# Kernel tuning notes

Hardware: AMD Instinct MI355X
Metric: run time of the kernel (lower is better)

Reference implementation:

```python
import jax, jax.numpy as jnp
import numpy as np

N_EMBED = 4096
N_Q_HEADS = 32
N_KV_HEADS = 8
HEAD_DIM = N_EMBED // N_Q_HEADS  # 128
N_GROUPS = N_Q_HEADS // N_KV_HEADS  # 4
ROPE_BASE = 10000.0
BATCH, SEQ = 1, 2048


def setup_inputs() -> dict:
    key = jax.random.key(0)
    ks = jax.random.split(key, 5)
    hidden_state = jax.random.normal(ks[0], (BATCH, SEQ, N_EMBED), dtype=jnp.float32)
    # additive causal mask: 0 on/below diagonal, -inf above (SDPA float-mask semantics)
    causal = jnp.tril(jnp.ones((SEQ, SEQ), dtype=bool))
    attention_mask = jnp.where(causal, 0.0, -jnp.inf).astype(jnp.float32)[None, None]
    position_ids = jnp.arange(SEQ, dtype=jnp.int32)[None, :].repeat(BATCH, axis=0)
    s = 0.02
    Wq = jax.random.normal(ks[1], (N_EMBED, N_EMBED), dtype=jnp.float32) * s
    Wk = jax.random.normal(ks[2], (N_KV_HEADS * HEAD_DIM, N_EMBED), dtype=jnp.float32) * s
    Wv = jax.random.normal(ks[3], (N_KV_HEADS * HEAD_DIM, N_EMBED), dtype=jnp.float32) * s
    Wo = jax.random.normal(ks[4], (N_EMBED, N_EMBED), dtype=jnp.float32) * s
    return {"hidden_state": hidden_state, "attention_mask": attention_mask,
            "position_ids": position_ids, "Wq": Wq, "Wk": Wk, "Wv": Wv, "Wo": Wo}


def _rope_tables(position_ids):
    # mimic torch: inv_freq built in fp16 then used as float
    exponent = (jnp.arange(0, HEAD_DIM, 2, dtype=jnp.float16) / HEAD_DIM)
    inv_freq = (1.0 / (ROPE_BASE ** exponent)).astype(jnp.float32)  # [hd/2]
    m = position_ids.astype(jnp.float32)  # [bs, seq]
    m_theta = m[:, :, None] * inv_freq[None, None, :]  # [bs, seq, hd/2]
    m_theta = jnp.concatenate([m_theta, m_theta], axis=-1)  # [bs, seq, hd]
    return jnp.cos(m_theta), jnp.sin(m_theta)


def _rotate_half(x):
    half = x.shape[-1] // 2
    return jnp.concatenate([-x[..., half:], x[..., :half]], axis=-1)


def reference(hidden_state, attention_mask, position_ids, Wq, Wk, Wv, Wo):
    bs, seq, _ = hidden_state.shape
    q = (hidden_state @ Wq.T).reshape(bs, seq, N_Q_HEADS, HEAD_DIM).transpose(0, 2, 1, 3)
    k = (hidden_state @ Wk.T).reshape(bs, seq, N_KV_HEADS, HEAD_DIM).transpose(0, 2, 1, 3)
    v = (hidden_state @ Wv.T).reshape(bs, seq, N_KV_HEADS, HEAD_DIM).transpose(0, 2, 1, 3)

    cos, sin = _rope_tables(position_ids)
    cos, sin = cos[:, None], sin[:, None]  # broadcast over heads
    q = q * cos + _rotate_half(q) * sin
    k = k * cos + _rotate_half(k) * sin

    # GQA: group query heads per KV head instead of materializing KV copies
    qg = q.reshape(bs, N_KV_HEADS, N_GROUPS, seq, HEAD_DIM)
    scale = 1.0 / jnp.sqrt(jnp.float32(HEAD_DIM))
    scores = jnp.einsum('bhgqd,bhkd->bhgqk', qg, k) * scale + attention_mask[:, :, None]
    probs = jax.nn.softmax(scores, axis=-1)
    attn = jnp.einsum('bhgqk,bhkd->bhgqd', probs, v)  # [bs, kvh, g, seq, hd]
    attn = attn.reshape(bs, N_Q_HEADS, seq, HEAD_DIM).transpose(0, 2, 1, 3).reshape(bs, seq, N_EMBED)
    return attn @ Wo.T
```

## Files before the change

### kernel.cpp

```cpp
#include <hip/hip_runtime.h>
#include <hip/hip_bf16.h>

#define SEQ 2048
#define LDQKV 6144

typedef __attribute__((ext_vector_type(8))) __bf16 bf16x8;
typedef __attribute__((ext_vector_type(4))) __bf16 bf16x4;
typedef __attribute__((ext_vector_type(4))) float f32x4;

__device__ __forceinline__ void gload_lds16(const void* g, void* l) {
  __builtin_amdgcn_global_load_lds((__attribute__((address_space(1))) void*)(g),
                                   (__attribute__((address_space(3))) void*)(l), 16, 0, 0);
}

struct CvtArgs {
  const float* src0; const float* src1; const float* src2; const float* src3; const float* src4;
  __bf16* dst0; __bf16* dst1; __bf16* dst2; __bf16* dst3; __bf16* dst4;
};
__global__ __launch_bounds__(256) void cvt_all(CvtArgs a) {
  int b = blockIdx.x;
  const float* s; __bf16* d; int boff;
  if (b < 8192)       { s = a.src0; d = a.dst0; boff = b; }
  else if (b < 24576) { s = a.src1; d = a.dst1; boff = b - 8192; }
  else if (b < 28672) { s = a.src2; d = a.dst2; boff = b - 24576; }
  else if (b < 32768) { s = a.src3; d = a.dst3; boff = b - 28672; }
  else                { s = a.src4; d = a.dst4; boff = b - 32768; }
  long i = ((long)boff * 256 + threadIdx.x) * 4;
  f32x4 v = *(const f32x4*)(s + i);
  bf16x4 o;
  #pragma unroll
  for (int j = 0; j < 4; ++j) o[j] = (__bf16)v[j];
  *(bf16x4*)(d + i) = o;
}

__global__ __launch_bounds__(256) void rope_tab_k(const int* __restrict__ pos,
                                                  float* __restrict__ tab) {
  int i = blockIdx.x * 256 + threadIdx.x;
  int s = i >> 6, j = i & 63;
  float p = (float)pos[s];
  float pw = powf(10000.0f, (float)j * (1.0f / 64.0f));
  _Float16 ph = (_Float16)pw;
  _Float16 ivh = (_Float16)(1.0f / (float)ph);
  float freq = (float)ivh;
  float th = p * freq;
  tab[i] = cosf(th);
  tab[SEQ * 64 + i] = sinf(th);
}

__global__ __launch_bounds__(256) void rope_apply_k(__bf16* __restrict__ qkv,
                                                    const float* __restrict__ tab) {
  int i = blockIdx.x * 256 + threadIdx.x;
  int dc = i & 7;
  int ht = (i >> 3) % 40;
  int s = i / 320;
  long col = (ht < 32) ? (long)ht * 128 : (long)4096 + (long)(ht - 32) * 128;
  __bf16* p = qkv + (long)s * LDQKV + col + dc * 8;
  bf16x8 lo = *(bf16x8*)p;
  bf16x8 hi = *(bf16x8*)(p + 64);
  const float* tc = tab + (long)s * 64 + dc * 8;
  const float* ts = tc + SEQ * 64;
  bf16x8 lo2, hi2;
  #pragma unroll
  for (int e = 0; e < 8; ++e) {
    float c = tc[e], sn = ts[e];
    float lv = (float)lo[e], hv = (float)hi[e];
    lo2[e] = (__bf16)(lv * c - hv * sn);
    hi2[e] = (__bf16)(hv * c + lv * sn);
  }
  *(bf16x8*)p = lo2;
  *(bf16x8*)(p + 64) = hi2;
}

template <bool OUT_BF16>
__global__ __launch_bounds__(256) void gemm_nt(const __bf16* __restrict__ A,
                                               const __bf16* __restrict__ B,
                                               void* __restrict__ C,
                                               int K, int ldc) {
  __shared__ __align__(16) __bf16 Al[8192];
  __shared__ __align__(16) __bf16 Bl[8192];
  const int tid = threadIdx.x;
  const int wave = tid >> 6, lane = tid & 63;
  const int l15 = lane & 15, l4 = lane >> 4;
  const int brow = blockIdx.x * 128, bcol = blockIdx.y * 128;
  const int wm = wave >> 1, wn = wave & 1;

  f32x4 acc[4][4] = {};

  for (int k0 = 0; k0 < K; k0 += 64) {
    __syncthreads();
    #pragma unroll
    for (int i = 0; i < 4; ++i) {
      int fo = i * 2048 + wave * 512 + lane * 8;
      int r = fo >> 6, c = fo & 63;
      int cs = c ^ ((r & 7) << 3);
      gload_lds16(A + (long)(brow + r) * K + k0 + cs, &Al[i * 2048 + wave * 512]);
      gload_lds16(B + (long)(bcol + r) * K + k0 + cs, &Bl[i * 2048 + wave * 512]);
    }
    __syncthreads();
    #pragma unroll
    for (int ks = 0; ks < 2; ++ks) {
      bf16x8 af[4], bfr[4];
      #pragma unroll
      for (int mi = 0; mi < 4; ++mi) {
        int r = wm * 64 + mi * 16 + l15;
        int c = ks * 32 + l4 * 8;
        af[mi] = *(const bf16x8*)&Al[r * 64 + (c ^ ((r & 7) << 3))];
      }
      #pragma unroll
      for (int ni = 0; ni < 4; ++ni) {
        int r = wn * 64 + ni * 16 + l15;
        int c = ks * 32 + l4 * 8;
        bfr[ni] = *(const bf16x8*)&Bl[r * 64 + (c ^ ((r & 7) << 3))];
      }
      #pragma unroll
      for (int mi = 0; mi < 4; ++mi)
        #pragma unroll
        for (int ni = 0; ni < 4; ++ni)
          acc[mi][ni] = __builtin_amdgcn_mfma_f32_16x16x32_bf16(af[mi], bfr[ni], acc[mi][ni], 0, 0, 0);
    }
  }
  #pragma unroll
  for (int mi = 0; mi < 4; ++mi)
    #pragma unroll
    for (int ni = 0; ni < 4; ++ni)
      #pragma unroll
      for (int j = 0; j < 4; ++j) {
        long rr = brow + wm * 64 + mi * 16 + l4 * 4 + j;
        long cc = bcol + wn * 64 + ni * 16 + l15;
        float v = acc[mi][ni][j];
        if (OUT_BF16) ((__bf16*)C)[rr * ldc + cc] = (__bf16)v;
        else          ((float*)C)[rr * ldc + cc] = v;
      }
}

__global__ __launch_bounds__(256) void flash_k(const __bf16* __restrict__ qkv,
                                               __bf16* __restrict__ ctx) {
  __shared__ __align__(16) __bf16 Kl[8192];
  __shared__ __align__(16) __bf16 Vt[8192];
  __shared__ __align__(16) __bf16 Pl[4][1024];

  const int bid = blockIdx.x;
  const int h = bid & 31;
  const int qt = 31 - (bid >> 5);
  const int kvh = h >> 2;
  const int q0 = qt * 64;
  const int tid = threadIdx.x, wave = tid >> 6, lane = tid & 63;
  const int l15 = lane & 15, l4 = lane >> 4;
  const int d2 = tid & 63, grp = tid >> 6;

  const __bf16* Qp = qkv + (long)h * 128;
  const __bf16* Kp = qkv + 4096 + (long)kvh * 128;
  const __bf16* Vp = qkv + 5120 + (long)kvh * 128;

  bf16x8 aq[4];
  {
    long qr = q0 + wave * 16 + l15;
    #pragma unroll
    for (int ks = 0; ks < 4; ++ks)
      aq[ks] = *(const bf16x8*)(Qp + qr * LDQKV + ks * 32 + l4 * 8);
  }
  f32x4 accO[8] = {};
  float lsum[4] = {0.f, 0.f, 0.f, 0.f};
  const float cexp = 0.08838834764831845f * 1.4426950408889634f;

  for (int kv0 = 0; kv0 <= q0; kv0 += 64) {
    __syncthreads();
    #pragma unroll
    for (int i = 0; i < 4; ++i) {
      int fo = i * 2048 + wave * 512 + lane * 8;
      int r = fo >> 7, c = fo & 127;
      int cs = c ^ ((r & 7) << 3);
      gload_lds16(Kp + (long)(kv0 + r) * LDQKV + cs, &Kl[i * 2048 + wave * 512]);
    }
    unsigned int vv[2][8];
    #pragma unroll
    for (int rep = 0; rep < 2; ++rep) {
      int cch = grp * 2 + rep;
      #pragma unroll
      for (int i = 0; i < 8; ++i)
        vv[rep][i] = *(const unsigned int*)(Vp + (long)(kv0 + cch * 8 + i) * LDQKV + 2 * d2);
    }
    #pragma unroll
    for (int rep = 0; rep < 2; ++rep) {
      int cch = grp * 2 + rep;
      #pragma unroll
      for (int half = 0; half < 2; ++half) {
        bf16x8 w;
        #pragma unroll
        for (int i = 0; i < 8; ++i)
          w[i] = __builtin_bit_cast(__bf16, (unsigned short)(vv[rep][i] >> (16 * half)));
        int d = 2 * d2 + half;
        *(bf16x8*)&Vt[d * 64 + ((cch * 8) ^ ((d2 & 7) * 8))] = w;
      }
    }
    __syncthreads();

    f32x4 s[4];
    #pragma unroll
    for (int t = 0; t < 4; ++t) s[t] = f32x4{0.f, 0.f, 0.f, 0.f};
    __builtin_amdgcn_s_setprio(1);
    #pragma unroll
    for (int t = 0; t < 4; ++t) {
      int r = t * 16 + l15;
      #pragma unroll
      for (int ks = 0; ks < 4; ++ks) {
        bf16x8 bk = *(const bf16x8*)&Kl[r * 128 + ((ks * 32 + l4 * 8) ^ ((r & 7) << 3))];
        s[t] = __builtin_amdgcn_mfma_f32_16x16x32_bf16(aq[ks], bk, s[t], 0, 0, 0);
      }
    }
    __builtin_amdgcn_s_setprio(0);

    const bool lastStep = (kv0 == q0);
    float pout[4][4];
    #pragma unroll
    for (int t = 0; t < 4; ++t)
      #pragma unroll
      for (int j = 0; j < 4; ++j) {
        float p = exp2f(s[t][j] * cexp);
        if (lastStep) {
          int qg = wave * 16 + l4 * 4 + j;
          int kg = t * 16 + l15;
          if (kg > qg) p = 0.f;
        }
        pout[t][j] = p;
      }
    #pragma unroll
    for (int j = 0; j < 4; ++j)
      lsum[j] += (pout[0][j] + pout[1][j]) + (pout[2][j] + pout[3][j]);

    #pragma unroll
    for (int t = 0; t < 4; ++t)
      #pragma unroll
      for (int j = 0; j < 4; ++j) {
        int r = l4 * 4 + j;
        int c = t * 16 + l15;
        Pl[wave][r * 64 + (c ^ ((r & 7) << 3))] = (__bf16)pout[t][j];
      }
    asm volatile("s_waitcnt lgkmcnt(0)" ::: "memory");
    __builtin_amdgcn_sched_barrier(0);
    bf16x8 ap[2];
    #pragma unroll
    for (int ks2 = 0; ks2 < 2; ++ks2) {
      int c = ks2 * 32 + l4 * 8;
      ap[ks2] = *(const bf16x8*)&Pl[wave][l15 * 64 + (c ^ ((l15 & 7) << 3))];
    }
    __builtin_amdgcn_s_setprio(1);
    #pragma unroll
    for (int dt = 0; dt < 8; ++dt) {
      int d = dt * 16 + l15;
      #pragma unroll
      for (int ks2 = 0; ks2 < 2; ++ks2) {
        int c = (ks2 * 32 + l4 * 8) ^ (((l15 >> 1) & 7) * 8);
        bf16x8 bv = *(const bf16x8*)&Vt[d * 64 + c];
        accO[dt] = __builtin_amdgcn_mfma_f32_16x16x32_bf16(ap[ks2], bv, accO[dt], 0, 0, 0);
      }
    }
    __builtin_amdgcn_s_setprio(0);
  }
  float rls[4];
  #pragma unroll
  for (int j = 0; j < 4; ++j) {
    float ls = lsum[j];
    ls += __shfl_xor(ls, 1, 16);
    ls += __shfl_xor(ls, 2, 16);
    ls += __shfl_xor(ls, 4, 16);
    ls += __shfl_xor(ls, 8, 16);
    rls[j] = 1.f / ls;
  }
  #pragma unroll
  for (int dt = 0; dt < 8; ++dt)
    #pragma unroll
    for (int j = 0; j < 4; ++j) {
      long qr = q0 + wave * 16 + l4 * 4 + j;
      long cc = (long)h * 128 + dt * 16 + l15;
      ctx[qr * 4096 + cc] = (__bf16)(accO[dt][j] * rls[j]);
    }
}

extern "C" void kernel_launch(void* const* d_in, const int* in_sizes, int n_in,
                              void* d_out, int out_size, void* d_ws, size_t ws_size,
                              hipStream_t stream) {
  const float* hs  = (const float*)d_in[0];
  const int*   pos = (const int*)d_in[2];
  const float* Wq  = (const float*)d_in[3];
  const float* Wk  = (const float*)d_in[4];
  const float* Wv  = (const float*)d_in[5];
  const float* Wo  = (const float*)d_in[6];
  char* ws = (char*)d_ws;
  __bf16* hsb  = (__bf16*)(ws + 0L);
  __bf16* wqkv = (__bf16*)(ws + 16777216L);
  __bf16* wob  = (__bf16*)(ws + 67108864L);
  __bf16* qkvb = (__bf16*)(ws + 100663296L);
  float*  tab  = (float*)(ws + 125829120L);
  __bf16* ctx  = (__bf16*)(ws + 126877696L);

  CvtArgs ca;
  ca.src0 = hs;  ca.dst0 = hsb;
  ca.src1 = Wq;  ca.dst1 = wqkv;
  ca.src2 = Wk;  ca.dst2 = wqkv + 16777216L;
  ca.src3 = Wv;  ca.dst3 = wqkv + 20971520L;
  ca.src4 = Wo;  ca.dst4 = wob;
  cvt_all<<<49152, 256, 0, stream>>>(ca);
  rope_tab_k<<<512, 256, 0, stream>>>(pos, tab);

  dim3 g1(16, 48);
  gemm_nt<true><<<g1, 256, 0, stream>>>(hsb, wqkv, qkvb, 4096, 6144);

  rope_apply_k<<<2560, 256, 0, stream>>>(qkvb, tab);

  flash_k<<<1024, 256, 0, stream>>>(qkvb, ctx);

  dim3 g2(16, 32);
  gemm_nt<false><<<g2, 256, 0, stream>>>(ctx, wob, d_out, 4096, 4096);
}
```

Baseline: 332.3 us.

## Replace GEMMs with 8-wave double-buffered ping-pong kernel using larger N tiles

```diff
diff --git a/kernel.cpp b/kernel.cpp
--- a/kernel.cpp
+++ b/kernel.cpp
@@ -71,66 +71,134 @@
   *(bf16x8*)(p + 64) = hi2;
 }
 
-template <bool OUT_BF16>
-__global__ __launch_bounds__(256) void gemm_nt(const __bf16* __restrict__ A,
-                                               const __bf16* __restrict__ B,
-                                               void* __restrict__ C,
-                                               int K, int ldc) {
-  __shared__ __align__(16) __bf16 Al[8192];
-  __shared__ __align__(16) __bf16 Bl[8192];
+template<int BN, bool OUT_BF16>
+__global__ __launch_bounds__(512, 2) void gemm8(const __bf16* __restrict__ A,
+                                                const __bf16* __restrict__ B,
+                                                void* __restrict__ C,
+                                                int K, int ldc) {
+  constexpr int BHR = BN / 2;
+  constexpr int NFR = BN / 128;
+  constexpr int LB  = BHR / 64;
+  constexpr int NW  = 1 + LB;
+  extern __shared__ __bf16 lds[];
+  __bf16* Ab = lds;
+  __bf16* Bb = lds + 16384;
+
   const int tid = threadIdx.x;
   const int wave = tid >> 6, lane = tid & 63;
   const int l15 = lane & 15, l4 = lane >> 4;
-  const int brow = blockIdx.x * 128, bcol = blockIdx.y * 128;
-  const int wm = wave >> 1, wn = wave & 1;
-
-  f32x4 acc[4][4] = {};
-
-  for (int k0 = 0; k0 < K; k0 += 64) {
-    __syncthreads();
-    #pragma unroll
-    for (int i = 0; i < 4; ++i) {
-      int fo = i * 2048 + wave * 512 + lane * 8;
-      int r = fo >> 6, c = fo & 63;
-      int cs = c ^ ((r & 7) << 3);
-      gload_lds16(A + (long)(brow + r) * K + k0 + cs, &Al[i * 2048 + wave * 512]);
-      gload_lds16(B + (long)(bcol + r) * K + k0 + cs, &Bl[i * 2048 + wave * 512]);
-    }
-    __syncthreads();
-    #pragma unroll
-    for (int ks = 0; ks < 2; ++ks) {
-      bf16x8 af[4], bfr[4];
-      #pragma unroll
-      for (int mi = 0; mi < 4; ++mi) {
-        int r = wm * 64 + mi * 16 + l15;
-        int c = ks * 32 + l4 * 8;
-        af[mi] = *(const bf16x8*)&Al[r * 64 + (c ^ ((r & 7) << 3))];
-      }
-      #pragma unroll
-      for (int ni = 0; ni < 4; ++ni) {
-        int r = wn * 64 + ni * 16 + l15;
-        int c = ks * 32 + l4 * 8;
-        bfr[ni] = *(const bf16x8*)&Bl[r * 64 + (c ^ ((r & 7) << 3))];
-      }
-      #pragma unroll
-      for (int mi = 0; mi < 4; ++mi)
+  const int wm = wave >> 2, wn = wave & 3;
+
+  const int orig = blockIdx.x;
+  const int swz = (orig & 7) * 32 + (orig >> 3);
+  const int bx = swz & 15, by = swz >> 4;
+  const long brow = (long)bx * 128, bcol = (long)by * BN;
+
+  const int rS = tid >> 3;
+  const int cS = ((tid & 7) * 8) ^ ((rS & 7) << 3);
+  const int NT = K >> 6;
+
+  auto stageA = [&](int buf, int qm, int t) {
+    const __bf16* src = A + (brow + qm * 64 + rS) * (long)K + t * 64 + cS;
+    gload_lds16(src, Ab + (buf * 2 + qm) * 4096 + wave * 512);
+  };
+  auto stageB = [&](int buf, int qn, int t) {
+    #pragma unroll
+    for (int i = 0; i < LB; ++i) {
+      const __bf16* src = B + (bcol + qn * BHR + i * 64 + rS) * (long)K + t * 64 + cS;
+      gload_lds16(src, Bb + (buf * 2 + qn) * (BHR * 64) + i * 4096 + wave * 512);
+    }
+  };
+
+  bf16x8 af[2][2], bfr[NFR][2];
+  auto readA = [&](int buf, int qm) {
+    #pragma unroll
+    for (int mi = 0; mi < 2; ++mi) {
+      int r = wm * 32 + mi * 16 + l15;
+      #pragma unroll
+      for (int kf = 0; kf < 2; ++kf) {
+        int c = (kf * 32 + l4 * 8) ^ ((r & 7) << 3);
+        af[mi][kf] = *(const bf16x8*)&Ab[(buf * 2 + qm) * 4096 + r * 64 + c];
+      }
+    }
+  };
+  auto readB = [&](int buf, int qn) {
+    #pragma unroll
+    for (int ni = 0; ni < NFR; ++ni) {
+      int r = wn * (BN / 8) + ni * 16 + l15;
+      #pragma unroll
+      for (int kf = 0; kf < 2; ++kf) {
+        int c = (kf * 32 + l4 * 8) ^ ((r & 7) << 3);
+        bfr[ni][kf] = *(const bf16x8*)&Bb[(buf * 2 + qn) * (BHR * 64) + r * 64 + c];
+      }
+    }
+  };
+
+  f32x4 acc[2][2][2][NFR] = {};
+  auto mfmaQ = [&](f32x4 (&ac)[2][NFR]) {
+    __builtin_amdgcn_s_setprio(1);
+    #pragma unroll
+    for (int mi = 0; mi < 2; ++mi)
+      #pragma unroll
+      for (int ni = 0; ni < NFR; ++ni)
         #pragma unroll
-        for (int ni = 0; ni < 4; ++ni)
-          acc[mi][ni] = __builtin_amdgcn_mfma_f32_16x16x32_bf16(af[mi], bfr[ni], acc[mi][ni], 0, 0, 0);
-    }
-  }
-  #pragma unroll
-  for (int mi = 0; mi < 4; ++mi)
-    #pragma unroll
-    for (int ni = 0; ni < 4; ++ni)
-      #pragma unroll
-      for (int j = 0; j < 4; ++j) {
-        long rr = brow + wm * 64 + mi * 16 + l4 * 4 + j;
-        long cc = bcol + wn * 64 + ni * 16 + l15;
-        float v = acc[mi][ni][j];
-        if (OUT_BF16) ((__bf16*)C)[rr * ldc + cc] = (__bf16)v;
-        else          ((float*)C)[rr * ldc + cc] = v;
-      }
+        for (int kf = 0; kf < 2; ++kf)
+          ac[mi][ni] = __builtin_amdgcn_mfma_f32_16x16x32_bf16(af[mi][kf], bfr[ni][kf], ac[mi][ni], 0, 0, 0);
+    __builtin_amdgcn_s_setprio(0);
+  };
+
+  #define VM_WAIT() do { \
+    if constexpr (NW == 4) asm volatile("s_waitcnt vmcnt(4)" ::: "memory"); \
+    else                   asm volatile("s_waitcnt vmcnt(3)" ::: "memory"); \
+  } while (0)
+  #define PH_BAR() do { __builtin_amdgcn_s_barrier(); __builtin_amdgcn_sched_barrier(0); } while (0)
+
+  stageA(0, 0, 0); stageB(0, 0, 0); stageA(0, 1, 0); stageB(0, 1, 0);
+  VM_WAIT();
+  PH_BAR();
+
+  for (int t = 0; t < NT; ++t) {
+    const int buf = t & 1, nb = buf ^ 1;
+    const bool pf = (t + 1 < NT);
+    if (pf) stageA(nb, 0, t + 1);
+    readA(buf, 0); readB(buf, 0);
+    mfmaQ(acc[0][0]);
+    VM_WAIT();
+    PH_BAR();
+    if (pf) stageB(nb, 0, t + 1);
+    readA(buf, 1);
+    mfmaQ(acc[1][0]);
+    VM_WAIT();
+    PH_BAR();
+    if (pf) stageA(nb, 1, t + 1);
+    readB(buf, 1);
+    mfmaQ(acc[1][1]);
+    PH_BAR();
+    if (pf) stageB(nb, 1, t + 1);
+    readA(buf, 0);
+    mfmaQ(acc[0][1]);
+    VM_WAIT();
+    PH_BAR();
+  }
+  #undef VM_WAIT
+  #undef PH_BAR
+
+  #pragma unroll
+  for (int qm = 0; qm < 2; ++qm)
+    #pragma unroll
+    for (int qn = 0; qn < 2; ++qn)
+      #pragma unroll
+      for (int mi = 0; mi < 2; ++mi)
+        #pragma unroll
+        for (int ni = 0; ni < NFR; ++ni)
+          #pragma unroll
+          for (int j = 0; j < 4; ++j) {
+            long rr = brow + qm * 64 + wm * 32 + mi * 16 + l4 * 4 + j;
+            long cc = bcol + qn * BHR + wn * (BN / 8) + ni * 16 + l15;
+            float v = acc[qm][qn][mi][ni][j];
+            if (OUT_BF16) ((__bf16*)C)[rr * ldc + cc] = (__bf16)v;
+            else          ((float*)C)[rr * ldc + cc] = v;
+          }
 }
 
 __global__ __launch_bounds__(256) void flash_k(const __bf16* __restrict__ qkv,
@@ -294,6 +362,11 @@
   float*  tab  = (float*)(ws + 125829120L);
   __bf16* ctx  = (__bf16*)(ws + 126877696L);
 
+  (void)hipFuncSetAttribute(reinterpret_cast<const void*>(&gemm8<384, true>),
+                            hipFuncAttributeMaxDynamicSharedMemorySize, 131072);
+  (void)hipFuncSetAttribute(reinterpret_cast<const void*>(&gemm8<256, false>),
+                            hipFuncAttributeMaxDynamicSharedMemorySize, 98304);
+
   CvtArgs ca;
   ca.src0 = hs;  ca.dst0 = hsb;
   ca.src1 = Wq;  ca.dst1 = wqkv;
@@ -303,13 +376,11 @@
   cvt_all<<<49152, 256, 0, stream>>>(ca);
   rope_tab_k<<<512, 256, 0, stream>>>(pos, tab);
 
-  dim3 g1(16, 48);
-  gemm_nt<true><<<g1, 256, 0, stream>>>(hsb, wqkv, qkvb, 4096, 6144);
+  gemm8<384, true><<<256, 512, 131072, stream>>>(hsb, wqkv, qkvb, 4096, 6144);
 
   rope_apply_k<<<2560, 256, 0, stream>>>(qkvb, tab);
 
   flash_k<<<1024, 256, 0, stream>>>(qkvb, ctx);
 
-  dim3 g2(16, 32);
-  gemm_nt<false><<<g2, 256, 0, stream>>>(ctx, wob, d_out, 4096, 4096);
-}
+  gemm8<256, false><<<256, 512, 98304, stream>>>(ctx, wob, d_out, 4096, 4096);
+}
```

After: 303.1 us. 8.8% less time.

## Replace GEMM with double-buffered 8-wave pipelined kernel with larger N tiles

Applied to the files above, without the earlier changes.

```diff
diff --git a/kernel.cpp b/kernel.cpp
--- a/kernel.cpp
+++ b/kernel.cpp
@@ -12,6 +12,8 @@
   __builtin_amdgcn_global_load_lds((__attribute__((address_space(1))) void*)(g),
                                    (__attribute__((address_space(3))) void*)(l), 16, 0, 0);
 }
+
+#define VMW(n) asm volatile("s_waitcnt vmcnt(" #n ")" ::: "memory")
 
 struct CvtArgs {
   const float* src0; const float* src1; const float* src2; const float* src3; const float* src4;
@@ -71,62 +73,117 @@
   *(bf16x8*)(p + 64) = hi2;
 }
 
-template <bool OUT_BF16>
-__global__ __launch_bounds__(256) void gemm_nt(const __bf16* __restrict__ A,
-                                               const __bf16* __restrict__ B,
-                                               void* __restrict__ C,
-                                               int K, int ldc) {
-  __shared__ __align__(16) __bf16 Al[8192];
-  __shared__ __align__(16) __bf16 Bl[8192];
+template<int BN, bool OUT_BF16>
+__global__ __launch_bounds__(512, 2) void gemm8p(const __bf16* __restrict__ A,
+                                                 const __bf16* __restrict__ B,
+                                                 void* __restrict__ C,
+                                                 int K, int ldc) {
+  constexpr int NI  = BN / 64;
+  constexpr int BCH = BN / 128;
+  constexpr int BOFF = 16384;
+  constexpr int BBUF = 2 * BN * 32;
+  extern __shared__ __bf16 lds[];
+
   const int tid = threadIdx.x;
   const int wave = tid >> 6, lane = tid & 63;
   const int l15 = lane & 15, l4 = lane >> 4;
-  const int brow = blockIdx.x * 128, bcol = blockIdx.y * 128;
-  const int wm = wave >> 1, wn = wave & 1;
-
-  f32x4 acc[4][4] = {};
-
-  for (int k0 = 0; k0 < K; k0 += 64) {
-    __syncthreads();
-    #pragma unroll
-    for (int i = 0; i < 4; ++i) {
-      int fo = i * 2048 + wave * 512 + lane * 8;
-      int r = fo >> 6, c = fo & 63;
-      int cs = c ^ ((r & 7) << 3);
-      gload_lds16(A + (long)(brow + r) * K + k0 + cs, &Al[i * 2048 + wave * 512]);
-      gload_lds16(B + (long)(bcol + r) * K + k0 + cs, &Bl[i * 2048 + wave * 512]);
-    }
-    __syncthreads();
-    #pragma unroll
-    for (int ks = 0; ks < 2; ++ks) {
-      bf16x8 af[4], bfr[4];
-      #pragma unroll
-      for (int mi = 0; mi < 4; ++mi) {
-        int r = wm * 64 + mi * 16 + l15;
-        int c = ks * 32 + l4 * 8;
-        af[mi] = *(const bf16x8*)&Al[r * 64 + (c ^ ((r & 7) << 3))];
-      }
-      #pragma unroll
-      for (int ni = 0; ni < 4; ++ni) {
-        int r = wn * 64 + ni * 16 + l15;
-        int c = ks * 32 + l4 * 8;
-        bfr[ni] = *(const bf16x8*)&Bl[r * 64 + (c ^ ((r & 7) << 3))];
-      }
-      #pragma unroll
-      for (int mi = 0; mi < 4; ++mi)
-        #pragma unroll
-        for (int ni = 0; ni < 4; ++ni)
-          acc[mi][ni] = __builtin_amdgcn_mfma_f32_16x16x32_bf16(af[mi], bfr[ni], acc[mi][ni], 0, 0, 0);
-    }
-  }
+  const int wm = wave >> 2, wn = wave & 3;
+
+  const int orig = blockIdx.x;
+  const int swz = (orig & 7) * 32 + (orig >> 3);
+  const int bx = swz & 15, by = swz >> 4;
+  const long brow = (long)bx * 128, bcol = (long)by * BN;
+
+  const int aRow = tid >> 3, aCol = ((tid & 7) ^ ((tid >> 3) & 7)) * 8;
+  const int bRow = tid >> 2, bCol = ((tid & 3) ^ ((tid >> 3) & 3)) * 8;
+  const int NT = K >> 6;
+
+  auto issue = [&](int nb, int idx, int t) {
+    if (idx < 2) {
+      gload_lds16(A + (brow + idx * 64 + aRow) * (long)K + t * 64 + aCol,
+                  lds + nb * 8192 + idx * 4096 + wave * 512);
+    } else {
+      const int kf = (idx - 2) / BCH, cb = (idx - 2) % BCH;
+      gload_lds16(B + (bcol + cb * 128 + bRow) * (long)K + t * 64 + kf * 32 + bCol,
+                  lds + BOFF + nb * BBUF + kf * (BN * 32) + cb * 4096 + wave * 512);
+    }
+  };
+
+  bf16x8 af[2], bfr[NI];
+  auto readA2 = [&](int buf, int kf, int mih) {
+    #pragma unroll
+    for (int m2 = 0; m2 < 2; ++m2) {
+      int r = wm * 64 + (mih * 2 + m2) * 16 + l15;
+      af[m2] = *(const bf16x8*)&lds[buf * 8192 + r * 64 + ((kf * 4 + l4) ^ (r & 7)) * 8];
+    }
+  };
+  auto readBN = [&](int buf, int kf) {
+    #pragma unroll
+    for (int ni = 0; ni < NI; ++ni) {
+      int r = wn * (NI * 16) + ni * 16 + l15;
+      int g = l4 ^ ((r >> 1) & 3);
+      bfr[ni] = *(const bf16x8*)&lds[BOFF + buf * BBUF + kf * (BN * 32) + r * 32 + g * 8];
+    }
+  };
+
+  f32x4 acc[4][NI] = {};
+  auto mfma2 = [&](int mih) {
+    __builtin_amdgcn_s_setprio(1);
+    #pragma unroll
+    for (int m2 = 0; m2 < 2; ++m2)
+      #pragma unroll
+      for (int ni = 0; ni < NI; ++ni)
+        acc[mih * 2 + m2][ni] =
+            __builtin_amdgcn_mfma_f32_16x16x32_bf16(af[m2], bfr[ni], acc[mih * 2 + m2][ni], 0, 0, 0);
+    __builtin_amdgcn_s_setprio(0);
+  };
+
+  #define PH_PRE()  do { __builtin_amdgcn_sched_barrier(0); __builtin_amdgcn_s_barrier(); \
+                         asm volatile("s_waitcnt lgkmcnt(0)" ::: "memory"); \
+                         __builtin_amdgcn_sched_barrier(0); } while (0)
+
+  #pragma unroll
+  for (int i = 0; i < 2 + 2 * BCH; ++i) issue(0, i, 0);
+  if constexpr (BCH == 3) VMW(3); else VMW(2);
+  __builtin_amdgcn_s_barrier();
+
+  for (int t = 0; t < NT; ++t) {
+    const int buf = t & 1, nb = buf ^ 1;
+    const bool pf = (t + 1 < NT);
+    const int t1 = t + 1;
+    readBN(buf, 0); readA2(buf, 0, 0);
+    if (pf) { issue(nb, 0, t1); issue(nb, 1, t1); }
+    PH_PRE();
+    mfma2(0);
+    __builtin_amdgcn_s_barrier();
+    readA2(buf, 0, 1);
+    if (pf) { issue(nb, 2, t1); issue(nb, 3, t1); }
+    PH_PRE();
+    mfma2(1);
+    if (pf) VMW(4); else VMW(0);
+    __builtin_amdgcn_s_barrier();
+    readBN(buf, 1); readA2(buf, 1, 0);
+    if (pf) { issue(nb, 4, t1); issue(nb, 5, t1); }
+    PH_PRE();
+    mfma2(0);
+    __builtin_amdgcn_s_barrier();
+    readA2(buf, 1, 1);
+    if (pf) { if constexpr (BCH == 3) { issue(nb, 6, t1); issue(nb, 7, t1); } }
+    PH_PRE();
+    mfma2(1);
+    if (pf) { if constexpr (BCH == 3) VMW(3); else VMW(2); }
+    __builtin_amdgcn_s_barrier();
+  }
+  #undef PH_PRE
+
   #pragma unroll
   for (int mi = 0; mi < 4; ++mi)
     #pragma unroll
-    for (int ni = 0; ni < 4; ++ni)
+    for (int ni = 0; ni < NI; ++ni)
       #pragma unroll
       for (int j = 0; j < 4; ++j) {
         long rr = brow + wm * 64 + mi * 16 + l4 * 4 + j;
-        long cc = bcol + wn * 64 + ni * 16 + l15;
+        long cc = bcol + wn * (NI * 16) + ni * 16 + l15;
         float v = acc[mi][ni][j];
         if (OUT_BF16) ((__bf16*)C)[rr * ldc + cc] = (__bf16)v;
         else          ((float*)C)[rr * ldc + cc] = v;
@@ -294,6 +351,11 @@
   float*  tab  = (float*)(ws + 125829120L);
   __bf16* ctx  = (__bf16*)(ws + 126877696L);
 
+  (void)hipFuncSetAttribute(reinterpret_cast<const void*>(&gemm8p<384, true>),
+                            hipFuncAttributeMaxDynamicSharedMemorySize, 131072);
+  (void)hipFuncSetAttribute(reinterpret_cast<const void*>(&gemm8p<256, false>),
+                            hipFuncAttributeMaxDynamicSharedMemorySize, 98304);
+
   CvtArgs ca;
   ca.src0 = hs;  ca.dst0 = hsb;
   ca.src1 = Wq;  ca.dst1 = wqkv;
@@ -303,13 +365,11 @@
   cvt_all<<<49152, 256, 0, stream>>>(ca);
   rope_tab_k<<<512, 256, 0, stream>>>(pos, tab);
 
-  dim3 g1(16, 48);
-  gemm_nt<true><<<g1, 256, 0, stream>>>(hsb, wqkv, qkvb, 4096, 6144);
+  gemm8p<384, true><<<256, 512, 131072, stream>>>(hsb, wqkv, qkvb, 4096, 6144);
 
   rope_apply_k<<<2560, 256, 0, stream>>>(qkvb, tab);
 
   flash_k<<<1024, 256, 0, stream>>>(qkvb, ctx);
 
-  dim3 g2(16, 32);
-  gemm_nt<false><<<g2, 256, 0, stream>>>(ctx, wob, d_out, 4096, 4096);
-}
+  gemm8p<256, false><<<256, 512, 98304, stream>>>(ctx, wob, d_out, 4096, 4096);
+}
```

After: 304.2 us. -8.5%, faster.

## Rewrite GEMMs as double-buffered 256-row tiles with interleaved load/MFMA schedule

Applied to the files above, without the earlier changes.

```diff
diff --git a/kernel.cpp b/kernel.cpp
--- a/kernel.cpp
+++ b/kernel.cpp
@@ -12,6 +12,11 @@
   __builtin_amdgcn_global_load_lds((__attribute__((address_space(1))) void*)(g),
                                    (__attribute__((address_space(3))) void*)(l), 16, 0, 0);
 }
+
+#define VMW(n) do { asm volatile("s_waitcnt vmcnt(" #n ")" ::: "memory"); \
+                    __builtin_amdgcn_sched_barrier(0); } while (0)
+#define SBAR() __builtin_amdgcn_sched_barrier(0)
+#define BAR()  __builtin_amdgcn_s_barrier()
 
 struct CvtArgs {
   const float* src0; const float* src1; const float* src2; const float* src3; const float* src4;
@@ -71,65 +76,124 @@
   *(bf16x8*)(p + 64) = hi2;
 }
 
-template <bool OUT_BF16>
-__global__ __launch_bounds__(256) void gemm_nt(const __bf16* __restrict__ A,
-                                               const __bf16* __restrict__ B,
-                                               void* __restrict__ C,
-                                               int K, int ldc) {
-  __shared__ __align__(16) __bf16 Al[8192];
-  __shared__ __align__(16) __bf16 Bl[8192];
+template<int BN, bool OUT_BF16>
+__global__ __launch_bounds__(512, 2) void gemmK(const __bf16* __restrict__ A,
+                                                const __bf16* __restrict__ B,
+                                                void* __restrict__ C,
+                                                int K, int ldc) {
+  constexpr int NF = BN / 64;
+  constexpr int LB = (BN * 64 * 2) / 8192;
+  extern __shared__ __bf16 lds[];
+  __bf16* Abuf = lds;
+  __bf16* Bbuf = lds + 32768;
+
   const int tid = threadIdx.x;
   const int wave = tid >> 6, lane = tid & 63;
   const int l15 = lane & 15, l4 = lane >> 4;
-  const int brow = blockIdx.x * 128, bcol = blockIdx.y * 128;
-  const int wm = wave >> 1, wn = wave & 1;
-
-  f32x4 acc[4][4] = {};
-
-  for (int k0 = 0; k0 < K; k0 += 64) {
-    __syncthreads();
-    #pragma unroll
-    for (int i = 0; i < 4; ++i) {
-      int fo = i * 2048 + wave * 512 + lane * 8;
-      int r = fo >> 6, c = fo & 63;
-      int cs = c ^ ((r & 7) << 3);
-      gload_lds16(A + (long)(brow + r) * K + k0 + cs, &Al[i * 2048 + wave * 512]);
-      gload_lds16(B + (long)(bcol + r) * K + k0 + cs, &Bl[i * 2048 + wave * 512]);
-    }
-    __syncthreads();
-    #pragma unroll
-    for (int ks = 0; ks < 2; ++ks) {
-      bf16x8 af[4], bfr[4];
-      #pragma unroll
-      for (int mi = 0; mi < 4; ++mi) {
-        int r = wm * 64 + mi * 16 + l15;
-        int c = ks * 32 + l4 * 8;
-        af[mi] = *(const bf16x8*)&Al[r * 64 + (c ^ ((r & 7) << 3))];
-      }
-      #pragma unroll
-      for (int ni = 0; ni < 4; ++ni) {
-        int r = wn * 64 + ni * 16 + l15;
-        int c = ks * 32 + l4 * 8;
-        bfr[ni] = *(const bf16x8*)&Bl[r * 64 + (c ^ ((r & 7) << 3))];
-      }
-      #pragma unroll
-      for (int mi = 0; mi < 4; ++mi)
-        #pragma unroll
-        for (int ni = 0; ni < 4; ++ni)
-          acc[mi][ni] = __builtin_amdgcn_mfma_f32_16x16x32_bf16(af[mi], bfr[ni], acc[mi][ni], 0, 0, 0);
-    }
-  }
-  #pragma unroll
-  for (int mi = 0; mi < 4; ++mi)
-    #pragma unroll
-    for (int ni = 0; ni < 4; ++ni)
+  const int wm = wave >> 2, wn = wave & 3;
+
+  const int orig = blockIdx.x;
+  const int swz = (orig & 7) * 32 + (orig >> 3);
+  const int bx = swz >> 5, by = swz & 31;
+  const long brow = (long)bx * 256, bcol = (long)by * BN;
+
+  const int rT = tid >> 3;
+  const int cT = (((tid & 7) ^ (rT & 7)) * 8);
+  const int NT = K >> 6;
+
+  auto stA = [&](int nb, int g, int t) {
+    #pragma unroll
+    for (int i = 0; i < 2; ++i) {
+      int row = g * 64 + i * 128 + rT;
+      gload_lds16(A + (brow + row) * (long)K + t * 64 + cT,
+                  Abuf + nb * 16384 + (g + 2 * i) * 4096 + wave * 512);
+    }
+  };
+  auto stB = [&](int nb, int t) {
+    #pragma unroll
+    for (int i = 0; i < LB; ++i) {
+      int row = i * 64 + rT;
+      gload_lds16(B + (bcol + row) * (long)K + t * 64 + cT,
+                  Bbuf + nb * (BN * 64) + i * 4096 + wave * 512);
+    }
+  };
+
+  bf16x8 afA[4], afB[4], bk0[NF], bk1[NF];
+  auto readA = [&](bf16x8 (&dst)[4], int buf, int mh, int kf) {
+    #pragma unroll
+    for (int m = 0; m < 4; ++m) {
+      int r = wm * 128 + mh * 64 + m * 16 + l15;
+      dst[m] = *(const bf16x8*)&Abuf[buf * 16384 + r * 64 + (((kf * 4 + l4) ^ (r & 7)) * 8)];
+    }
+  };
+  auto readB = [&](bf16x8 (&dst)[NF], int buf, int kf) {
+    #pragma unroll
+    for (int n = 0; n < NF; ++n) {
+      int r = wn * (NF * 16) + n * 16 + l15;
+      dst[n] = *(const bf16x8*)&Bbuf[buf * (BN * 64) + r * 64 + (((kf * 4 + l4) ^ (r & 7)) * 8)];
+    }
+  };
+
+  f32x4 accLo[4][NF] = {}, accHi[4][NF] = {};
+  auto mfmaQ = [&](bf16x8 (&af)[4], bf16x8 (&bk)[NF], f32x4 (&ac)[4][NF]) {
+    __builtin_amdgcn_s_setprio(1);
+    #pragma unroll
+    for (int m = 0; m < 4; ++m)
+      #pragma unroll
+      for (int n = 0; n < NF; ++n)
+        ac[m][n] = __builtin_amdgcn_mfma_f32_16x16x32_bf16(af[m], bk[n], ac[m][n], 0, 0, 0);
+    __builtin_amdgcn_s_setprio(0);
+  };
+
+  stA(0, 0, 0); stB(0, 0); stA(0, 1, 0);
+  VMW(0);
+  BAR();
+  readA(afA, 0, 0, 0); readB(bk0, 0, 0);
+  SBAR();
+
+  for (int t = 0; t < NT; ++t) {
+    const int buf = t & 1, nb = buf ^ 1;
+    const bool pf = (t + 1 < NT);
+    const int t1 = t + 1;
+    if (pf) stA(nb, 0, t1);
+    readA(afB, buf, 1, 0);
+    SBAR(); BAR();
+    mfmaQ(afA, bk0, accLo);
+    SBAR(); BAR();
+    if (pf) stB(nb, t1);
+    readA(afA, buf, 1, 1); readB(bk1, buf, 1);
+    SBAR(); BAR();
+    mfmaQ(afB, bk0, accHi);
+    SBAR(); BAR();
+    if (pf) stA(nb, 1, t1);
+    readA(afB, buf, 0, 1);
+    SBAR(); BAR();
+    mfmaQ(afA, bk1, accHi);
+    VMW(2);
+    BAR();
+    if (pf) { readA(afA, nb, 0, 0); readB(bk0, nb, 0); }
+    SBAR(); BAR();
+    mfmaQ(afB, bk1, accLo);
+    VMW(0);
+    BAR();
+  }
+
+  #pragma unroll
+  for (int m = 0; m < 4; ++m)
+    #pragma unroll
+    for (int n = 0; n < NF; ++n)
       #pragma unroll
       for (int j = 0; j < 4; ++j) {
-        long rr = brow + wm * 64 + mi * 16 + l4 * 4 + j;
-        long cc = bcol + wn * 64 + ni * 16 + l15;
-        float v = acc[mi][ni][j];
-        if (OUT_BF16) ((__bf16*)C)[rr * ldc + cc] = (__bf16)v;
-        else          ((float*)C)[rr * ldc + cc] = v;
+        long rr = brow + wm * 128 + m * 16 + l4 * 4 + j;
+        long cc = bcol + wn * (NF * 16) + n * 16 + l15;
+        float vlo = accLo[m][n][j], vhi = accHi[m][n][j];
+        if (OUT_BF16) {
+          ((__bf16*)C)[rr * ldc + cc] = (__bf16)vlo;
+          ((__bf16*)C)[(rr + 64) * ldc + cc] = (__bf16)vhi;
+        } else {
+          ((float*)C)[rr * ldc + cc] = vlo;
+          ((float*)C)[(rr + 64) * ldc + cc] = vhi;
+        }
       }
 }
 
@@ -294,6 +358,11 @@
   float*  tab  = (float*)(ws + 125829120L);
   __bf16* ctx  = (__bf16*)(ws + 126877696L);
 
+  (void)hipFuncSetAttribute(reinterpret_cast<const void*>(&gemmK<192, true>),
+                            hipFuncAttributeMaxDynamicSharedMemorySize, 114688);
+  (void)hipFuncSetAttribute(reinterpret_cast<const void*>(&gemmK<128, false>),
+                            hipFuncAttributeMaxDynamicSharedMemorySize, 98304);
+
   CvtArgs ca;
   ca.src0 = hs;  ca.dst0 = hsb;
   ca.src1 = Wq;  ca.dst1 = wqkv;
@@ -303,13 +372,11 @@
   cvt_all<<<49152, 256, 0, stream>>>(ca);
   rope_tab_k<<<512, 256, 0, stream>>>(pos, tab);
 
-  dim3 g1(16, 48);
-  gemm_nt<true><<<g1, 256, 0, stream>>>(hsb, wqkv, qkvb, 4096, 6144);
+  gemmK<192, true><<<256, 512, 114688, stream>>>(hsb, wqkv, qkvb, 4096, 6144);
 
   rope_apply_k<<<2560, 256, 0, stream>>>(qkvb, tab);
 
   flash_k<<<1024, 256, 0, stream>>>(qkvb, ctx);
 
-  dim3 g2(16, 32);
-  gemm_nt<false><<<g2, 256, 0, stream>>>(ctx, wob, d_out, 4096, 4096);
-}
+  gemmK<128, false><<<256, 512, 98304, stream>>>(ctx, wob, d_out, 4096, 4096);
+}
```

Result: faster. 314.4 us (-5.4%).
